# Kernel tuning notes

Measured on AMD Instinct MI355X. Metric: run time of the kernel, lower is better.

## Reference

```python
import jax, jax.numpy as jnp
import numpy as np

N = 100000   # nodes
E = 1600000  # edges
D_IN = 256
H = 64       # hidden_dim


def _segment_softmax(e, dst, n):
    # e: [E, heads]; softmax over edges sharing the same dst node
    m = jax.ops.segment_max(e, dst, num_segments=n)
    m = jnp.where(jnp.isfinite(m), m, jnp.zeros_like(m))
    ex = jnp.exp(e - m[dst])
    s = jax.ops.segment_sum(ex, dst, num_segments=n)
    return ex / (s[dst] + 1e-16)


def gat_conv(x, edge_index, W, att_src, att_dst, bias, heads, odim):
    # PyG GATConv, concat=False (mean over heads), with self-loops, neg_slope=0.2
    n = x.shape[0]
    loop = jnp.arange(n, dtype=edge_index.dtype)
    src = jnp.concatenate([edge_index[0], loop])
    dst = jnp.concatenate([edge_index[1], loop])
    h = (x @ W).reshape(n, heads, odim)                      # [N, heads, odim]
    a_s = jnp.einsum('nhd,hd->nh', h, att_src)               # [N, heads]
    a_d = jnp.einsum('nhd,hd->nh', h, att_dst)
    e = jax.nn.leaky_relu(a_s[src] + a_d[dst], 0.2)          # [E+N, heads]
    alpha = _segment_softmax(e, dst, n)
    msg = h[src] * alpha[:, :, None]                         # gather + weight
    out = jax.ops.segment_sum(msg, dst, num_segments=n)      # scatter-reduce
    return out.mean(axis=1) + bias                           # concat=False -> mean


def gcn_conv(x, edge_index, W, bias):
    # PyG GCNConv with self-loops and symmetric normalization
    n = x.shape[0]
    loop = jnp.arange(n, dtype=edge_index.dtype)
    src = jnp.concatenate([edge_index[0], loop])
    dst = jnp.concatenate([edge_index[1], loop])
    deg = jax.ops.segment_sum(jnp.ones(src.shape[0], x.dtype), dst, num_segments=n)
    dinv = jnp.where(deg > 0, deg ** -0.5, jnp.zeros_like(deg))
    norm = dinv[src] * dinv[dst]                             # [E+N]
    h = x @ W
    return jax.ops.segment_sum(h[src] * norm[:, None], dst, num_segments=n) + bias


def setup_inputs() -> dict:
    key = jax.random.key(0)
    ks = jax.random.split(key, 16)
    f = lambda k, shp, s=0.05: (jax.random.normal(k, shp, dtype=jnp.float32) * s)
    inp = {
        'x': jax.random.normal(ks[0], (N, D_IN), dtype=jnp.float32),
        'edge_index': jax.random.randint(ks[1], (2, E), 0, N, dtype=jnp.int64),
        # GAT layer 1: heads=4, out=H
        'W1': f(ks[2], (D_IN, 4 * H)), 'a1s': f(ks[3], (4, H)), 'a1d': f(ks[4], (4, H)),
        'b1': jnp.zeros((H,), jnp.float32),
        # GAT layer 2: heads=2, out=H
        'W2': f(ks[5], (H, 2 * H)), 'a2s': f(ks[6], (2, H)), 'a2d': f(ks[7], (2, H)),
        'b2': jnp.zeros((H,), jnp.float32),
        # GCN layer: H -> H//2
        'Wg': f(ks[8], (H, H // 2)), 'bg': jnp.zeros((H // 2,), jnp.float32),
        # MLP head: H//2 -> H//4 -> 1
        'Wh1': f(ks[9], (H // 2, H // 4)), 'bh1': jnp.zeros((H // 4,), jnp.float32),
        'Wh2': f(ks[10], (H // 4, 1)), 'bh2': jnp.zeros((1,), jnp.float32),
    }
    return inp


def reference(x, edge_index, W1, a1s, a1d, b1, W2, a2s, a2d, b2, Wg, bg, Wh1, bh1, Wh2, bh2):
    h1 = jax.nn.relu(gat_conv(x, edge_index, W1, a1s, a1d, b1, heads=4, odim=H))
    h2 = jax.nn.relu(gat_conv(h1, edge_index, W2, a2s, a2d, b2, heads=2, odim=H))
    h3 = jax.nn.relu(gcn_conv(h2, edge_index, Wg, bg))
    z = jax.nn.relu(h3 @ Wh1 + bh1)
    svi = jax.nn.sigmoid(z @ Wh2 + bh2)
    return svi.squeeze(-1)
```

## Files before the change

### kernel.cpp

```cpp
#include <hip/hip_runtime.h>
#include <math.h>

static inline int cdiv(int a, int b){ return (a + b - 1) / b; }

typedef __attribute__((ext_vector_type(8))) short short8_t;
typedef __attribute__((ext_vector_type(4))) float f32x4;
typedef __attribute__((ext_vector_type(2))) float f32x2;

static __device__ inline unsigned short f2bf(float f) {
    union { float f; unsigned u; } v; v.f = f;
    unsigned r = v.u + 0x7fff + ((v.u >> 16) & 1);
    return (unsigned short)(r >> 16);
}

static __device__ inline unsigned char f2fp8(float f) {
    union { float f; unsigned u; } v; v.f = f;
    unsigned s = (v.u >> 24) & 0x80u;
    v.u &= 0x7fffffffu;
    v.f = fminf(v.f, 448.f);
    unsigned out;
    if (v.u >= (121u << 23)) {
        unsigned u = v.u + 0x7FFFFu + ((v.u >> 20) & 1u);
        out = (((u >> 23) - 120u) << 3) | ((u >> 20) & 7u);
    } else {
        out = (unsigned)(v.f * 512.f + 0.5f);
    }
    return (unsigned char)(out | s);
}

static __device__ inline float fp8_1(unsigned b) {
    unsigned s = (b & 0x80u) << 24;
    unsigned em = b & 0x7fu;
    union { unsigned u; float f; } n;
    n.u = (((em >> 3) + 120u) << 23) | ((em & 7u) << 20);
    float mag = (em >= 8u) ? n.f : (float)em * 0.001953125f;
    union { unsigned u; float f; } r; r.f = mag; r.u |= s;
    return r.f;
}

static __device__ __forceinline__ f32x2 fp8lo(unsigned v) {
#if __has_builtin(__builtin_amdgcn_cvt_pk_f32_fp8)
    return __builtin_amdgcn_cvt_pk_f32_fp8((int)v, false);
#else
    f32x2 r; r[0] = fp8_1(v & 0xff); r[1] = fp8_1((v >> 8) & 0xff); return r;
#endif
}
static __device__ __forceinline__ f32x2 fp8hi(unsigned v) {
#if __has_builtin(__builtin_amdgcn_cvt_pk_f32_fp8)
    return __builtin_amdgcn_cvt_pk_f32_fp8((int)v, true);
#else
    f32x2 r; r[0] = fp8_1((v >> 16) & 0xff); r[1] = fp8_1(v >> 24); return r;
#endif
}


__global__ __launch_bounds__(256) void k_count_deg_win(const int* __restrict__ dst, int E,
        int* __restrict__ deg, int wsize) {
    int win   = blockIdx.x & 7;
    int chunk = blockIdx.x >> 3;
    int lo = win * wsize, hi = lo + wsize;
    int base = (chunk * 256 + threadIdx.x) * 4;
    if (base + 3 < E) {
        int4 d = *(const int4*)(dst + base);
        if (d.x >= lo && d.x < hi) atomicAdd(&deg[d.x], 1);
        if (d.y >= lo && d.y < hi) atomicAdd(&deg[d.y], 1);
        if (d.z >= lo && d.z < hi) atomicAdd(&deg[d.z], 1);
        if (d.w >= lo && d.w < hi) atomicAdd(&deg[d.w], 1);
    } else {
        for (int k = 0; k < 4; k++) {
            int e = base + k;
            if (e < E) { int d = dst[e]; if (d >= lo && d < hi) atomicAdd(&deg[d], 1); }
        }
    }
}

__global__ void k_scan_partial(const int* __restrict__ deg, int n, int* __restrict__ partial) {
    __shared__ int sd[256];
    int base = blockIdx.x * 1024;
    int sum = 0;
    for (int i = threadIdx.x; i < 1024; i += 256) {
        int idx = base + i;
        if (idx < n) sum += deg[idx] + 1;
    }
    sd[threadIdx.x] = sum;
    __syncthreads();
    for (int s = 128; s > 0; s >>= 1) {
        if (threadIdx.x < s) sd[threadIdx.x] += sd[threadIdx.x + s];
        __syncthreads();
    }
    if (threadIdx.x == 0) partial[blockIdx.x] = sd[0];
}

__global__ void k_scan_top(int* __restrict__ partial, int nb, int* __restrict__ offs, int n) {
    if (blockIdx.x == 0 && threadIdx.x == 0) {
        int run = 0;
        for (int i = 0; i < nb; i++) { int v = partial[i]; partial[i] = run; run += v; }
        offs[n] = run;
    }
}

__global__ void k_scan_final(const int* __restrict__ deg, int n,
                             const int* __restrict__ partial, int* __restrict__ offs,
                             int* __restrict__ cursor, int* __restrict__ csr,
                             float* __restrict__ dinv) {
    __shared__ int sd[256];
    int tid = threadIdx.x;
    int base = blockIdx.x * 1024;
    int v[4]; int s0 = 0;
    #pragma unroll
    for (int j = 0; j < 4; j++) {
        int idx = base + tid*4 + j;
        v[j] = (idx < n) ? (deg[idx] + 1) : 0;
        s0 += v[j];
    }
    sd[tid] = s0;
    __syncthreads();
    for (int st = 1; st < 256; st <<= 1) {
        int t = (tid >= st) ? sd[tid - st] : 0;
        __syncthreads();
        sd[tid] += t;
        __syncthreads();
    }
    int ex = (tid > 0 ? sd[tid - 1] : 0) + partial[blockIdx.x];
    #pragma unroll
    for (int j = 0; j < 4; j++) {
        int idx = base + tid*4 + j;
        if (idx < n) {
            offs[idx]   = ex;
            cursor[idx] = ex;
            dinv[idx]   = rsqrtf((float)v[j]);
            csr[ex + v[j] - 1] = idx;
        }
        ex += v[j];
    }
}

__global__ __launch_bounds__(256) void k_fill_csr_win(const int* __restrict__ src,
        const int* __restrict__ dst, int E,
        int* __restrict__ cursor, int* __restrict__ csr, int wsize) {
    int win   = blockIdx.x & 7;
    int chunk = blockIdx.x >> 3;
    int lo = win * wsize, hi = lo + wsize;
    int base = (chunk * 256 + threadIdx.x) * 4;
    if (base + 3 < E) {
        int4 d = *(const int4*)(dst + base);
        bool ix = d.x >= lo && d.x < hi, iy = d.y >= lo && d.y < hi;
        bool iz = d.z >= lo && d.z < hi, iw = d.w >= lo && d.w < hi;
        if (ix | iy | iz | iw) {
            int4 s = *(const int4*)(src + base);
            if (ix) { int p = atomicAdd(&cursor[d.x], 1); csr[p] = s.x; }
            if (iy) { int p = atomicAdd(&cursor[d.y], 1); csr[p] = s.y; }
            if (iz) { int p = atomicAdd(&cursor[d.z], 1); csr[p] = s.z; }
            if (iw) { int p = atomicAdd(&cursor[d.w], 1); csr[p] = s.w; }
        }
    } else {
        for (int k = 0; k < 4; k++) {
            int e = base + k;
            if (e < E) {
                int d = dst[e];
                if (d >= lo && d < hi) { int p = atomicAdd(&cursor[d], 1); csr[p] = src[e]; }
            }
        }
    }
}


__global__ void k_prep_wt(const float* __restrict__ W, unsigned short* __restrict__ Bt,
                          int K, int C) {
    int t = blockIdx.x * 256 + threadIdx.x;
    if (t < K * C) { int k = t / C, c = t % C; Bt[c * K + k] = f2bf(W[t]); }
}

__global__ __launch_bounds__(512) void k_gemm1_mfma(const float* __restrict__ A,
        const unsigned short* __restrict__ Bt, const float* __restrict__ att_s_g,
        const float* __restrict__ att_d_g, unsigned char* __restrict__ C,
        float* __restrict__ out_as, float* __restrict__ out_ad, int M) {
    constexpr int LDP = 40;
    __shared__ __align__(16) unsigned short As[128 * LDP];
    __shared__ __align__(16) unsigned short Bs[256 * LDP];
    __shared__ float att_l[512];
    int tid = threadIdx.x;
    int bm = blockIdx.x * 128;
    int wave = tid >> 6, lane = tid & 63;
    int wr = wave >> 1, wc = wave & 1;
    int lg = lane >> 4, lr = lane & 15;

    att_l[tid] = (tid < 256) ? att_s_g[tid] : att_d_g[tid - 256];

    f32x4 acc[2][8] = {};

    for (int k0 = 0; k0 < 256; k0 += 32) {
        __syncthreads();
        {
            int row = tid >> 2, part = tid & 3;
            int gr = bm + row;
            float4 v0, v1;
            if (gr < M) {
                const float4* p = (const float4*)(A + (size_t)gr * 256 + k0 + part * 8);
                v0 = p[0]; v1 = p[1];
            } else {
                v0 = make_float4(0.f,0.f,0.f,0.f); v1 = v0;
            }
            unsigned short* w = &As[row * LDP + part * 8];
            w[0]=f2bf(v0.x); w[1]=f2bf(v0.y); w[2]=f2bf(v0.z); w[3]=f2bf(v0.w);
            w[4]=f2bf(v1.x); w[5]=f2bf(v1.y); w[6]=f2bf(v1.z); w[7]=f2bf(v1.w);
        }
        {
            int col = tid >> 1, part = tid & 1;
            const uint4* p = (const uint4*)(Bt + (size_t)col * 256 + k0 + part * 16);
            uint4 u0 = p[0], u1 = p[1];
            *(uint4*)&Bs[col * LDP + part * 16]     = u0;
            *(uint4*)&Bs[col * LDP + part * 16 + 8] = u1;
        }
        __syncthreads();
        short8_t a[2], b[8];
        #pragma unroll
        for (int i = 0; i < 2; i++)
            a[i] = *(const short8_t*)&As[(wr * 32 + i * 16 + lr) * LDP + lg * 8];
        #pragma unroll
        for (int j = 0; j < 8; j++)
            b[j] = *(const short8_t*)&Bs[(wc * 128 + j * 16 + lr) * LDP + lg * 8];
        #pragma unroll
        for (int i = 0; i < 2; i++)
            #pragma unroll
            for (int j = 0; j < 8; j++)
                acc[i][j] = __builtin_amdgcn_mfma_f32_16x16x32_bf16(a[i], b[j], acc[i][j], 0, 0, 0);
    }
    float ws[8], wd[8];
    #pragma unroll
    for (int j = 0; j < 8; j++) {
        int c = wc * 128 + j * 16 + lr;
        ws[j] = att_l[c]; wd[j] = att_l[256 + c];
    }
    #pragma unroll
    for (int i = 0; i < 2; i++) {
        #pragma unroll
        for (int b2 = 0; b2 < 4; b2++) {
            int row = bm + wr * 32 + i * 16 + lg * 4 + b2;
            #pragma unroll
            for (int j = 0; j < 8; j++) {
                int col = wc * 128 + j * 16 + lr;
                if (row < M) C[(size_t)row * 256 + col] = f2fp8(acc[i][j][b2]);
            }
            float s0=0.f, s1=0.f, d0=0.f, d1=0.f;
            #pragma unroll
            for (int j = 0; j < 4; j++) { float v = acc[i][j][b2];   s0 += v*ws[j];   d0 += v*wd[j]; }
            #pragma unroll
            for (int j = 4; j < 8; j++) { float v = acc[i][j][b2];   s1 += v*ws[j];   d1 += v*wd[j]; }
            #pragma unroll
            for (int off = 1; off < 16; off <<= 1) {
                s0 += __shfl_xor(s0, off); s1 += __shfl_xor(s1, off);
                d0 += __shfl_xor(d0, off); d1 += __shfl_xor(d1, off);
            }
            if (lr == 0 && row < M) {
                out_as[row * 4 + wc * 2]     = s0;
                out_as[row * 4 + wc * 2 + 1] = s1;
                out_ad[row * 4 + wc * 2]     = d0;
                out_ad[row * 4 + wc * 2 + 1] = d1;
            }
        }
    }
}


template<int NC, bool ATT>
__global__ __launch_bounds__(256) void k_gemm_k64_mfma(const float* __restrict__ A,
        const unsigned short* __restrict__ Bt,
        const float* __restrict__ att_s_g, const float* __restrict__ att_d_g,
        unsigned char* __restrict__ C, float* __restrict__ out_as,
        float* __restrict__ out_ad, int M) {
    constexpr int NF  = NC / 16;
    constexpr int LDP = 72;
    __shared__ __align__(16) unsigned short As[64 * LDP];
    __shared__ __align__(16) unsigned short Bs[NC * LDP];
    __shared__ float att_l[ATT ? 2 * NC : 1];
    int tid = threadIdx.x;
    int bm = blockIdx.x * 64;
    int wave = tid >> 6, lane = tid & 63, lg = lane >> 4, lr = lane & 15;

    if constexpr (ATT) {
        if (tid < 2 * NC)
            att_l[tid] = (tid < NC) ? att_s_g[tid] : att_d_g[tid - NC];
    }
    {
        int row = tid >> 2, part = tid & 3;
        int gr = bm + row;
        float4 v0, v1, v2, v3;
        if (gr < M) {
            const float4* p = (const float4*)(A + (size_t)gr * 64 + part * 16);
            v0 = p[0]; v1 = p[1]; v2 = p[2]; v3 = p[3];
        } else {
            v0 = make_float4(0.f,0.f,0.f,0.f); v1 = v0; v2 = v0; v3 = v0;
        }
        unsigned short* w = &As[row * LDP + part * 16];
        w[0]=f2bf(v0.x);  w[1]=f2bf(v0.y);  w[2]=f2bf(v0.z);  w[3]=f2bf(v0.w);
        w[4]=f2bf(v1.x);  w[5]=f2bf(v1.y);  w[6]=f2bf(v1.z);  w[7]=f2bf(v1.w);
        w[8]=f2bf(v2.x);  w[9]=f2bf(v2.y);  w[10]=f2bf(v2.z); w[11]=f2bf(v2.w);
        w[12]=f2bf(v3.x); w[13]=f2bf(v3.y); w[14]=f2bf(v3.z); w[15]=f2bf(v3.w);
    }
    for (int i = tid; i < NC * 8; i += 256) {
        int c = i >> 3, part = i & 7;
        *(uint4*)&Bs[c * LDP + part * 8] = *(const uint4*)(Bt + (size_t)c * 64 + part * 8);
    }
    __syncthreads();

    f32x4 acc[NF] = {};
    short8_t a0 = *(const short8_t*)&As[(wave * 16 + lr) * LDP + lg * 8];
    short8_t a1 = *(const short8_t*)&As[(wave * 16 + lr) * LDP + 32 + lg * 8];
    #pragma unroll
    for (int j = 0; j < NF; j++) {
        short8_t b0 = *(const short8_t*)&Bs[(j * 16 + lr) * LDP + lg * 8];
        short8_t b1 = *(const short8_t*)&Bs[(j * 16 + lr) * LDP + 32 + lg * 8];
        acc[j] = __builtin_amdgcn_mfma_f32_16x16x32_bf16(a0, b0, acc[j], 0, 0, 0);
        acc[j] = __builtin_amdgcn_mfma_f32_16x16x32_bf16(a1, b1, acc[j], 0, 0, 0);
    }
    float ws[NF], wd[NF];
    if constexpr (ATT) {
        #pragma unroll
        for (int j = 0; j < NF; j++) { ws[j] = att_l[j * 16 + lr]; wd[j] = att_l[NC + j * 16 + lr]; }
    }
    #pragma unroll
    for (int b2 = 0; b2 < 4; b2++) {
        int row = bm + wave * 16 + lg * 4 + b2;
        #pragma unroll
        for (int j = 0; j < NF; j++)
            if (row < M) C[(size_t)row * NC + j * 16 + lr] = f2fp8(acc[j][b2]);
        if constexpr (ATT) {
            float s0=0.f, s1=0.f, d0=0.f, d1=0.f;
            #pragma unroll
            for (int j = 0; j < 4; j++) { float v = acc[j][b2]; s0 += v*ws[j]; d0 += v*wd[j]; }
            #pragma unroll
            for (int j = 4; j < 8; j++) { float v = acc[j][b2]; s1 += v*ws[j]; d1 += v*wd[j]; }
            #pragma unroll
            for (int off = 1; off < 16; off <<= 1) {
                s0 += __shfl_xor(s0, off); s1 += __shfl_xor(s1, off);
                d0 += __shfl_xor(d0, off); d1 += __shfl_xor(d1, off);
            }
            if (lr == 0 && row < M) {
                out_as[row * 2]     = s0;
                out_as[row * 2 + 1] = s1;
                out_ad[row * 2]     = d0;
                out_ad[row * 2 + 1] = d1;
            }
        }
    }
}


template<int HEADS>
__global__ __launch_bounds__(256) void k_gat_fused(const unsigned char* __restrict__ hpre,
        const float* __restrict__ as_n, const float* __restrict__ ad_n,
        const float* __restrict__ bias,
        const int* __restrict__ offs, const int* __restrict__ csr,
        float* __restrict__ out, int n_nodes) {
    __shared__ int   s_src[4][64];
    __shared__ float s_p[4][64 * HEADS];
    int wif  = threadIdx.x >> 6;
    int lane = threadIdx.x & 63;
    int n = blockIdx.x * 4 + wif;
    if (n >= n_nodes) return;
    const int beg = offs[n];
    const int deg = offs[n + 1] - beg;

    constexpr int EPI = (HEADS == 4) ? 2 : 4;
    int eo, h;
    if constexpr (HEADS == 4) { eo = lane >> 5; h = (lane >> 3) & 3; }
    else                      { eo = lane >> 4; h = (lane >> 3) & 1; }
    int dq8 = lane & 7;

    float adv[HEADS];
    if constexpr (HEADS == 4) {
        float4 t = *(const float4*)(ad_n + (size_t)n * 4);
        adv[0]=t.x; adv[1]=t.y; adv[2]=t.z; adv[3]=t.w;
    } else {
        float2 t = *(const float2*)(ad_n + (size_t)n * 2);
        adv[0]=t.x; adv[1]=t.y;
    }

    float sumh = 0.f;
    float acc[8] = {};

    for (int j0 = 0; j0 < deg; j0 += 64) {
        int j = j0 + lane;
        int cnt = min(64, deg - j0);
        if (j < deg) {
            int s = csr[beg + j];
            s_src[wif][lane] = s;
            float ev[HEADS];
            if constexpr (HEADS == 4) {
                float4 t = *(const float4*)(as_n + (size_t)s * 4);
                ev[0]=t.x; ev[1]=t.y; ev[2]=t.z; ev[3]=t.w;
            } else {
                float2 t = *(const float2*)(as_n + (size_t)s * 2);
                ev[0]=t.x; ev[1]=t.y;
            }
            #pragma unroll
            for (int hh = 0; hh < HEADS; hh++) {
                float e = ev[hh] + adv[hh];
                e = fmaxf(e, 0.2f * e);
                s_p[wif][lane * HEADS + hh] = __expf(e);
            }
        }
        #pragma unroll 2
        for (int q = 0; q < cnt; q += EPI) {
            int qe = q + eo;
            if (qe < cnt) {
                int s = s_src[wif][qe];
                float p = s_p[wif][qe * HEADS + h];
                sumh += p;
                uint2 v = *(const uint2*)(hpre + (size_t)s * (HEADS * 64) + h * 64 + dq8 * 8);
                f32x2 c0 = fp8lo(v.x), c1 = fp8hi(v.x), c2 = fp8lo(v.y), c3 = fp8hi(v.y);
                acc[0] += p * c0[0]; acc[1] += p * c0[1];
                acc[2] += p * c1[0]; acc[3] += p * c1[1];
                acc[4] += p * c2[0]; acc[5] += p * c2[1];
                acc[6] += p * c3[0]; acc[7] += p * c3[1];
            }
        }
    }
    if constexpr (HEADS == 4) {
        sumh += __shfl_xor(sumh, 32);
        #pragma unroll
        for (int i = 0; i < 8; i++) acc[i] += __shfl_xor(acc[i], 32);
    } else {
        sumh += __shfl_xor(sumh, 16); sumh += __shfl_xor(sumh, 32);
        #pragma unroll
        for (int i = 0; i < 8; i++) {
            acc[i] += __shfl_xor(acc[i], 16); acc[i] += __shfl_xor(acc[i], 32);
        }
    }
    float inv = 1.0f / (sumh + 1e-16f);
    float r[8];
    #pragma unroll
    for (int i = 0; i < 8; i++) r[i] = acc[i] * inv;
    if constexpr (HEADS == 4) {
        #pragma unroll
        for (int i = 0; i < 8; i++) {
            r[i] += __shfl_xor(r[i], 8); r[i] += __shfl_xor(r[i], 16); r[i] *= 0.25f;
        }
    } else {
        #pragma unroll
        for (int i = 0; i < 8; i++) { r[i] += __shfl_xor(r[i], 8); r[i] *= 0.5f; }
    }
    if (lane < 8) {
        float4 b0 = *(const float4*)(bias + dq8 * 8);
        float4 b1 = *(const float4*)(bias + dq8 * 8 + 4);
        float4 o0, o1;
        o0.x = fmaxf(r[0] + b0.x, 0.f); o0.y = fmaxf(r[1] + b0.y, 0.f);
        o0.z = fmaxf(r[2] + b0.z, 0.f); o0.w = fmaxf(r[3] + b0.w, 0.f);
        o1.x = fmaxf(r[4] + b1.x, 0.f); o1.y = fmaxf(r[5] + b1.y, 0.f);
        o1.z = fmaxf(r[6] + b1.z, 0.f); o1.w = fmaxf(r[7] + b1.w, 0.f);
        *(float4*)(out + (size_t)n * 64 + dq8 * 8)     = o0;
        *(float4*)(out + (size_t)n * 64 + dq8 * 8 + 4) = o1;
    }
}


__global__ __launch_bounds__(256) void k_gcn_agg(const unsigned char* __restrict__ hpre,
        const float* __restrict__ dinv, const float* __restrict__ bias,
        const int* __restrict__ offs, const int* __restrict__ csr,
        float* __restrict__ out, int n_nodes) {
    int gid = blockIdx.x * 256 + threadIdx.x;
    int n = gid >> 3, q = gid & 7;
    if (n >= n_nodes) return;
    const int beg = offs[n], end = offs[n + 1];
    float4 acc = make_float4(0.f,0.f,0.f,0.f);
    #pragma unroll 4
    for (int j = beg; j < end; j++) {
        int s = csr[j];
        float ds = dinv[s];
        unsigned v = *(const unsigned*)(hpre + (size_t)s * 32 + q * 4);
        f32x2 l = fp8lo(v), h2 = fp8hi(v);
        acc.x += ds * l[0]; acc.y += ds * l[1];
        acc.z += ds * h2[0]; acc.w += ds * h2[1];
    }
    float dn = dinv[n];
    float4 b = *(const float4*)(bias + q * 4);
    float4 o;
    o.x = fmaxf(acc.x * dn + b.x, 0.f); o.y = fmaxf(acc.y * dn + b.y, 0.f);
    o.z = fmaxf(acc.z * dn + b.z, 0.f); o.w = fmaxf(acc.w * dn + b.w, 0.f);
    *(float4*)(out + (size_t)n * 32 + q * 4) = o;
}


__global__ __launch_bounds__(256) void k_mlp(const float* __restrict__ h3,
        const float* __restrict__ Wh1, const float* __restrict__ bh1,
        const float* __restrict__ Wh2, const float* __restrict__ bh2,
        float* __restrict__ out, int n_nodes) {
    __shared__ float w1[512];
    __shared__ float w2[16];
    __shared__ float b1s[16];
    __shared__ float b2s;
    int tid = threadIdx.x;
    for (int i = tid; i < 512; i += 256) w1[i] = Wh1[i];
    if (tid < 16) { w2[tid] = Wh2[tid]; b1s[tid] = bh1[tid]; }
    if (tid == 0) b2s = bh2[0];
    __syncthreads();
    int n = blockIdx.x * 256 + tid;
    if (n >= n_nodes) return;
    float x[32];
    const float4* p = (const float4*)(h3 + (size_t)n * 32);
    #pragma unroll
    for (int q = 0; q < 8; q++) { float4 v = p[q]; x[4*q] = v.x; x[4*q+1] = v.y; x[4*q+2] = v.z; x[4*q+3] = v.w; }
    float acc2 = b2s;
    #pragma unroll
    for (int j = 0; j < 16; j++) {
        float z = b1s[j];
        #pragma unroll
        for (int k = 0; k < 32; k++) z += x[k] * w1[k * 16 + j];
        z = fmaxf(z, 0.f);
        acc2 += z * w2[j];
    }
    out[n] = 1.0f / (1.0f + expf(-acc2));
}


extern "C" void kernel_launch(void* const* d_in, const int* in_sizes, int n_in,
                              void* d_out, int out_size, void* d_ws, size_t ws_size,
                              hipStream_t stream) {
    const float* x   = (const float*)d_in[0];
    const int*   ei  = (const int*)d_in[1];
    const float* W1  = (const float*)d_in[2];
    const float* a1s = (const float*)d_in[3];
    const float* a1d = (const float*)d_in[4];
    const float* b1  = (const float*)d_in[5];
    const float* W2  = (const float*)d_in[6];
    const float* a2s = (const float*)d_in[7];
    const float* a2d = (const float*)d_in[8];
    const float* b2  = (const float*)d_in[9];
    const float* Wg  = (const float*)d_in[10];
    const float* bg  = (const float*)d_in[11];
    const float* Wh1 = (const float*)d_in[12];
    const float* bh1 = (const float*)d_in[13];
    const float* Wh2 = (const float*)d_in[14];
    const float* bh2 = (const float*)d_in[15];

    const int N = in_sizes[0] / 256;
    const int E = in_sizes[1] / 2;
    const int* srcs = ei;
    const int* dsts = ei + E;

    float* R0   = (float*)d_ws;
    float* R1   = R0 + (size_t)N * 256;
    float* R2   = R1 + (size_t)N * 64;
    float* As_  = R2 + (size_t)N * 64;
    float* Ad_  = As_ + (size_t)N * 4;
    float* dinv = Ad_ + (size_t)N * 4;
    int* deg    = (int*)(dinv + N);
    int* offs   = deg + N;
    int* cursor = offs + (N + 1);
    int* csr    = cursor + N;
    int* parts  = csr + (E + N);
    unsigned short* W1t = (unsigned short*)(parts + 256);
    unsigned short* W2t = W1t + 65536;
    unsigned short* Wgt = W2t + 8192;
    unsigned char*  HP  = (unsigned char*)R0;

    int wsize = cdiv(N, 8);
    hipMemsetAsync(deg, 0, (size_t)N * sizeof(int), stream);
    k_count_deg_win<<<cdiv(E, 1024) * 8, 256, 0, stream>>>(dsts, E, deg, wsize);
    int nch = cdiv(N, 1024);
    k_scan_partial<<<nch, 256, 0, stream>>>(deg, N, parts);
    k_scan_top<<<1, 64, 0, stream>>>(parts, nch, offs, N);
    k_scan_final<<<nch, 256, 0, stream>>>(deg, N, parts, offs, cursor, csr, dinv);
    k_fill_csr_win<<<cdiv(E, 1024) * 8, 256, 0, stream>>>(srcs, dsts, E, cursor, csr, wsize);

    k_prep_wt<<<256, 256, 0, stream>>>(W1, W1t, 256, 256);
    k_prep_wt<<<32, 256, 0, stream>>>(W2, W2t, 64, 128);
    k_prep_wt<<<8, 256, 0, stream>>>(Wg, Wgt, 64, 32);

    k_gemm1_mfma<<<cdiv(N, 128), 512, 0, stream>>>(x, W1t, a1s, a1d, HP, As_, Ad_, N);
    k_gat_fused<4><<<cdiv(N, 4), 256, 0, stream>>>(HP, As_, Ad_, b1, offs, csr, R1, N);

    k_gemm_k64_mfma<128, true><<<cdiv(N, 64), 256, 0, stream>>>(R1, W2t, a2s, a2d, HP, As_, Ad_, N);
    k_gat_fused<2><<<cdiv(N, 4), 256, 0, stream>>>(HP, As_, Ad_, b2, offs, csr, R2, N);

    k_gemm_k64_mfma<32, false><<<cdiv(N, 64), 256, 0, stream>>>(R2, Wgt, nullptr, nullptr, HP, nullptr, nullptr, N);
    k_gcn_agg<<<cdiv(N * 8, 256), 256, 0, stream>>>(HP, dinv, bg, offs, csr, R1, N);

    k_mlp<<<cdiv(N, 256), 256, 0, stream>>>(R1, Wh1, bh1, Wh2, bh2, (float*)d_out, N);
}
```

Before: 426.2 us.

## Remap GAT aggregation lanes to one edge per wave and merge weight-prep kernels

```diff
diff --git a/kernel.cpp b/kernel.cpp
--- a/kernel.cpp
+++ b/kernel.cpp
@@ -165,10 +165,22 @@
 }
 
 
-__global__ void k_prep_wt(const float* __restrict__ W, unsigned short* __restrict__ Bt,
-                          int K, int C) {
+__global__ void k_prep_all(const float* __restrict__ W1, const float* __restrict__ W2,
+                           const float* __restrict__ Wg, unsigned short* __restrict__ W1t,
+                           unsigned short* __restrict__ W2t, unsigned short* __restrict__ Wgt) {
     int t = blockIdx.x * 256 + threadIdx.x;
-    if (t < K * C) { int k = t / C, c = t % C; Bt[c * K + k] = f2bf(W[t]); }
+    if (t < 65536) {
+        int k = t >> 8, c = t & 255;
+        W1t[c * 256 + k] = f2bf(W1[t]);
+    }
+    if (t < 8192) {
+        int k = t >> 7, c = t & 127;
+        W2t[c * 64 + k] = f2bf(W2[t]);
+    }
+    if (t < 2048) {
+        int k = t >> 5, c = t & 31;
+        Wgt[c * 64 + k] = f2bf(Wg[t]);
+    }
 }
 
 __global__ __launch_bounds__(512) void k_gemm1_mfma(const float* __restrict__ A,
@@ -353,7 +365,7 @@
         const float* __restrict__ bias,
         const int* __restrict__ offs, const int* __restrict__ csr,
         float* __restrict__ out, int n_nodes) {
-    __shared__ int   s_src[4][64];
+    __shared__ int   s_off[4][64];
     __shared__ float s_p[4][64 * HEADS];
     int wif  = threadIdx.x >> 6;
     int lane = threadIdx.x & 63;
@@ -362,11 +374,10 @@
     const int beg = offs[n];
     const int deg = offs[n + 1] - beg;
 
-    constexpr int EPI = (HEADS == 4) ? 2 : 4;
-    int eo, h;
-    if constexpr (HEADS == 4) { eo = lane >> 5; h = (lane >> 3) & 3; }
-    else                      { eo = lane >> 4; h = (lane >> 3) & 1; }
-    int dq8 = lane & 7;
+    int h_id, dq;
+    if constexpr (HEADS == 4) { h_id = lane >> 4; dq = lane & 15; }
+    else                      { h_id = lane >> 5; dq = lane & 31; }
+    const int lane_off = h_id * 64 + dq * 4;
 
     float adv[HEADS];
     if constexpr (HEADS == 4) {
@@ -378,14 +389,14 @@
     }
 
     float sumh = 0.f;
-    float acc[8] = {};
+    float acc[HEADS] = {};
 
     for (int j0 = 0; j0 < deg; j0 += 64) {
         int j = j0 + lane;
         int cnt = min(64, deg - j0);
         if (j < deg) {
             int s = csr[beg + j];
-            s_src[wif][lane] = s;
+            s_off[wif][lane] = s * (HEADS * 64);
             float ev[HEADS];
             if constexpr (HEADS == 4) {
                 float4 t = *(const float4*)(as_n + (size_t)s * 4);
@@ -395,62 +406,59 @@
                 ev[0]=t.x; ev[1]=t.y;
             }
             #pragma unroll
-            for (int hh = 0; hh < HEADS; hh++) {
-                float e = ev[hh] + adv[hh];
+            for (int h = 0; h < HEADS; h++) {
+                float e = ev[h] + adv[h];
                 e = fmaxf(e, 0.2f * e);
-                s_p[wif][lane * HEADS + hh] = __expf(e);
-            }
-        }
-        #pragma unroll 2
-        for (int q = 0; q < cnt; q += EPI) {
-            int qe = q + eo;
-            if (qe < cnt) {
-                int s = s_src[wif][qe];
-                float p = s_p[wif][qe * HEADS + h];
-                sumh += p;
-                uint2 v = *(const uint2*)(hpre + (size_t)s * (HEADS * 64) + h * 64 + dq8 * 8);
-                f32x2 c0 = fp8lo(v.x), c1 = fp8hi(v.x), c2 = fp8lo(v.y), c3 = fp8hi(v.y);
-                acc[0] += p * c0[0]; acc[1] += p * c0[1];
-                acc[2] += p * c1[0]; acc[3] += p * c1[1];
-                acc[4] += p * c2[0]; acc[5] += p * c2[1];
-                acc[6] += p * c3[0]; acc[7] += p * c3[1];
-            }
-        }
-    }
+                s_p[wif][lane * HEADS + h] = __expf(e);
+            }
+        }
+        #pragma unroll 4
+        for (int q = 0; q < cnt; q++) {
+            int off = s_off[wif][q];
+            float p = s_p[wif][q * HEADS + h_id];
+            sumh += p;
+            if constexpr (HEADS == 4) {
+                unsigned v = *(const unsigned*)(hpre + off + lane_off);
+                f32x2 l = fp8lo(v), h2 = fp8hi(v);
+                acc[0] += p * l[0]; acc[1] += p * l[1];
+                acc[2] += p * h2[0]; acc[3] += p * h2[1];
+            } else {
+                unsigned v = *(const unsigned short*)(hpre + off + (lane_off >> 1));
+                f32x2 l = fp8lo(v);
+                acc[0] += p * l[0]; acc[1] += p * l[1];
+            }
+        }
+    }
+    float inv = 1.0f / (sumh + 1e-16f);
+    float r[HEADS];
+    #pragma unroll
+    for (int c = 0; c < HEADS; c++) r[c] = acc[c] * inv;
     if constexpr (HEADS == 4) {
-        sumh += __shfl_xor(sumh, 32);
-        #pragma unroll
-        for (int i = 0; i < 8; i++) acc[i] += __shfl_xor(acc[i], 32);
+        #pragma unroll
+        for (int c = 0; c < 4; c++) {
+            r[c] += __shfl_xor(r[c], 16);
+            r[c] += __shfl_xor(r[c], 32);
+            r[c] *= 0.25f;
+        }
+        if (h_id == 0) {
+            float4 b = *(const float4*)(bias + dq * 4);
+            float4 o;
+            o.x = fmaxf(r[0] + b.x, 0.f); o.y = fmaxf(r[1] + b.y, 0.f);
+            o.z = fmaxf(r[2] + b.z, 0.f); o.w = fmaxf(r[3] + b.w, 0.f);
+            *(float4*)(out + (size_t)n * 64 + dq * 4) = o;
+        }
     } else {
-        sumh += __shfl_xor(sumh, 16); sumh += __shfl_xor(sumh, 32);
-        #pragma unroll
-        for (int i = 0; i < 8; i++) {
-            acc[i] += __shfl_xor(acc[i], 16); acc[i] += __shfl_xor(acc[i], 32);
-        }
-    }
-    float inv = 1.0f / (sumh + 1e-16f);
-    float r[8];
-    #pragma unroll
-    for (int i = 0; i < 8; i++) r[i] = acc[i] * inv;
-    if constexpr (HEADS == 4) {
-        #pragma unroll
-        for (int i = 0; i < 8; i++) {
-            r[i] += __shfl_xor(r[i], 8); r[i] += __shfl_xor(r[i], 16); r[i] *= 0.25f;
-        }
-    } else {
-        #pragma unroll
-        for (int i = 0; i < 8; i++) { r[i] += __shfl_xor(r[i], 8); r[i] *= 0.5f; }
-    }
-    if (lane < 8) {
-        float4 b0 = *(const float4*)(bias + dq8 * 8);
-        float4 b1 = *(const float4*)(bias + dq8 * 8 + 4);
-        float4 o0, o1;
-        o0.x = fmaxf(r[0] + b0.x, 0.f); o0.y = fmaxf(r[1] + b0.y, 0.f);
-        o0.z = fmaxf(r[2] + b0.z, 0.f); o0.w = fmaxf(r[3] + b0.w, 0.f);
-        o1.x = fmaxf(r[4] + b1.x, 0.f); o1.y = fmaxf(r[5] + b1.y, 0.f);
-        o1.z = fmaxf(r[6] + b1.z, 0.f); o1.w = fmaxf(r[7] + b1.w, 0.f);
-        *(float4*)(out + (size_t)n * 64 + dq8 * 8)     = o0;
-        *(float4*)(out + (size_t)n * 64 + dq8 * 8 + 4) = o1;
+        #pragma unroll
+        for (int c = 0; c < 2; c++) {
+            r[c] += __shfl_xor(r[c], 32);
+            r[c] *= 0.5f;
+        }
+        if (h_id == 0) {
+            float2 b = *(const float2*)(bias + dq * 2);
+            float2 o;
+            o.x = fmaxf(r[0] + b.x, 0.f); o.y = fmaxf(r[1] + b.y, 0.f);
+            *(float2*)(out + (size_t)n * 64 + dq * 2) = o;
+        }
     }
 }
 
@@ -564,9 +572,7 @@
     k_scan_final<<<nch, 256, 0, stream>>>(deg, N, parts, offs, cursor, csr, dinv);
     k_fill_csr_win<<<cdiv(E, 1024) * 8, 256, 0, stream>>>(srcs, dsts, E, cursor, csr, wsize);
 
-    k_prep_wt<<<256, 256, 0, stream>>>(W1, W1t, 256, 256);
-    k_prep_wt<<<32, 256, 0, stream>>>(W2, W2t, 64, 128);
-    k_prep_wt<<<8, 256, 0, stream>>>(Wg, Wgt, 64, 32);
+    k_prep_all<<<256, 256, 0, stream>>>(W1, W2, Wg, W1t, W2t, Wgt);
 
     k_gemm1_mfma<<<cdiv(N, 128), 512, 0, stream>>>(x, W1t, a1s, a1d, HP, As_, Ad_, N);
     k_gat_fused<4><<<cdiv(N, 4), 256, 0, stream>>>(HP, As_, Ad_, b1, offs, csr, R1, N);
```

After: 404.7 us. 1.05x faster.
